# Kernel optimization log

Measured on AMD Instinct MI355X. Metric: run time of the kernel, lower is better.

The kernel has to match this reference:

```python
import jax, jax.numpy as jnp
import numpy as np

N_QUBITS = 14
CPLX = jnp.complex64


def _simulate(x, params):
    """Batched state-vector simulation of the QuantumGate circuit.

    x: (B, n) float angles for RX encoding; params: (2*n,) shared RY angles.
    Returns (B, n) Pauli-Z expectations.
    """
    n = N_QUBITS
    B = x.shape[0]
    dim = 2 ** n

    # RX(theta)|0> = [cos(theta/2), -i sin(theta/2)] per qubit -> product state.
    half = 0.5 * x
    c = jnp.cos(half).astype(CPLX)          # (B, n)
    s = jnp.sin(half).astype(CPLX)
    v = jnp.stack([c, -1j * s], axis=-1)     # (B, n, 2)

    state = jnp.ones((B, 1), dtype=CPLX)
    for q in range(n):  # fixed small loop over qubits; builds (B, 2^n)
        state = (state[:, :, None] * v[:, q, None, :]).reshape(B, -1)

    p = params.reshape(2, n)
    for layer in range(2):
        # RY rotations (shared angles across batch)
        for w in range(n):
            th = 0.5 * p[layer, w]
            cw, sw = jnp.cos(th), jnp.sin(th)
            G = jnp.stack([jnp.stack([cw, -sw]), jnp.stack([sw, cw])]).astype(CPLX)  # 2x2
            left, right = 2 ** w, 2 ** (n - w - 1)
            st = state.reshape(B, left, 2, right)
            state = jnp.einsum('ij,bljr->blir', G, st).reshape(B, dim)
        # CNOT chain on adjacent wires (w -> w+1)
        for w in range(n - 1):
            left, right = 2 ** w, 2 ** (n - w - 2)
            st = state.reshape(B, left, 2, 2, right)
            st = jnp.concatenate([st[:, :, 0:1], st[:, :, 1:2, ::-1]], axis=2)
            state = st.reshape(B, dim)

    probs = state.real ** 2 + state.imag ** 2  # (B, 2^n)
    outs = []
    for w in range(n):
        left, right = 2 ** w, 2 ** (n - w - 1)
        pr = probs.reshape(B, left, 2, right)
        outs.append(pr[:, :, 0].sum(axis=(1, 2)) - pr[:, :, 1].sum(axis=(1, 2)))
    return jnp.stack(outs, axis=1)  # (B, n)


def setup_inputs() -> dict:
    key = jax.random.key(0)
    k1, k2 = jax.random.split(key)
    x = jax.random.normal(k1, (4096, N_QUBITS), dtype=jnp.float32)
    params = jax.random.normal(k2, (2 * N_QUBITS,), dtype=jnp.float32)
    return {"x": x, "params": params}


def reference(x, params):
    return _simulate(x, params)
```

## Files before the change

### kernel.cpp

```cpp
#include <hip/hip_runtime.h>
#include <hip/hip_bf16.h>

#define NQ 14
#define BLOCK 64
#define ELEMS_PER_BLOCK (BLOCK / 8)


typedef float2 cplx;
__device__ __forceinline__ cplx cmul(cplx a, cplx b) {
    return make_float2(a.x * b.x - a.y * b.y, a.x * b.y + a.y * b.x);
}
__device__ __forceinline__ cplx cmadd(cplx acc, cplx a, cplx b) {
    return make_float2(acc.x + a.x * b.x - a.y * b.y,
                       acc.y + a.x * b.y + a.y * b.x);
}
__device__ __forceinline__ cplx conjc(cplx a) { return make_float2(a.x, -a.y); }
__device__ __forceinline__ cplx cscale(float s, cplx a) { return make_float2(s * a.x, s * a.y); }

__global__ __launch_bounds__(BLOCK) void qsim_tm(const void* __restrict__ xraw,
                                                 const void* __restrict__ praw,
                                                 void* __restrict__ outraw)
{
    const int tid  = threadIdx.x;
    const int lane = tid & 63;
    const int s    = lane & 7;
    const int g8   = lane & ~7;
    const int e  = (s >> 2) & 1;
    const int d  = (s >> 1) & 1;
    const int dp = s & 1;
    const int b  = blockIdx.x * ELEMS_PER_BLOCK + (tid >> 3);

    const unsigned short* hw = (const unsigned short*)xraw;
    int ev = 0;
    for (int k = 0; k < 64; ++k) {
        unsigned short v = hw[k];
        int ex = (v >> 7) & 0xFF;
        if (ex == 0xFF || ex > 140 || (ex != 0 && ex < 110)) ev++;
    }
    const int isbf = (ev < 8) ? 1 : 0;

    float c1a[NQ], s1a[NQ];
    cplx u0[NQ], u1[NQ];
    #pragma unroll
    for (int q = 0; q < NQ; ++q) {
        float p0, p1, xq;
        if (isbf) {
            p0 = (float)((const __hip_bfloat16*)praw)[q];
            p1 = (float)((const __hip_bfloat16*)praw)[NQ + q];
            xq = (float)((const __hip_bfloat16*)xraw)[b * NQ + q];
        } else {
            p0 = ((const float*)praw)[q];
            p1 = ((const float*)praw)[NQ + q];
            xq = ((const float*)xraw)[b * NQ + q];
        }
        float c0 = cosf(0.5f * p0), s0 = sinf(0.5f * p0);
        c1a[q] = cosf(0.5f * p1);
        s1a[q] = sinf(0.5f * p1);
        float rc = cosf(0.5f * xq), rs = sinf(0.5f * xq);
        u0[q] = make_float2(c0 * rc,  s0 * rs);
        u1[q] = make_float2(s0 * rc, -c0 * rs);
    }

    cplx L = make_float2((s == 0) ? 1.0f : 0.0f, 0.0f);
    cplx hist[NQ];
    #pragma unroll
    for (int q = 0; q < NQ; ++q) {
        float Lr[8], Li[8];
        #pragma unroll
        for (int sp = 0; sp < 8; ++sp) {
            Lr[sp] = __shfl(L.x, g8 + sp, 64);
            Li[sp] = __shfl(L.y, g8 + sp, 64);
        }
        const float c1 = c1a[q], s1 = s1a[q];
        const float gd0 = d  ? -s1 : c1;
        const float gd1 = d  ?  c1 : s1;
        const float gp0 = dp ? -s1 : c1;
        const float gp1 = dp ?  c1 : s1;
        const cplx ud    = d  ? u1[q] : u0[q];
        const cplx udx   = d  ? u0[q] : u1[q];
        const cplx updc  = conjc(dp ? u1[q] : u0[q]);
        const cplx updxc = conjc(dp ? u0[q] : u1[q]);

        cplx newL = make_float2(0.0f, 0.0f);
        #pragma unroll
        for (int ep = 0; ep < 2; ++ep) {
            const int f = e ^ ep;
            const float gg = (f == 0) ? (gd0 * gp0) : (gd1 * gp1);
            const int base = ep << 2;
            cplx in0 = cmadd(cmul(updc, make_float2(Lr[base + 0], Li[base + 0])),
                             updxc, make_float2(Lr[base + 1], Li[base + 1]));
            cplx in1 = cmadd(cmul(updc, make_float2(Lr[base + 2], Li[base + 2])),
                             updxc, make_float2(Lr[base + 3], Li[base + 3]));
            cplx mid = cmadd(cmul(ud, in0), udx, in1);
            newL = cmadd(newL, make_float2(gg, 0.0f), mid);
        }
        L = newL;
        hist[q] = L;
    }

    const float sgn = e ? -1.0f : 1.0f;
    cplx R = make_float2(1.0f, 0.0f);
    #pragma unroll
    for (int qq = 0; qq < NQ; ++qq) {
        const int q = NQ - 1 - qq;
        float t = sgn * (hist[q].x * R.x - hist[q].y * R.y);
        t += __shfl_xor(t, 1, 64);
        t += __shfl_xor(t, 2, 64);
        t += __shfl_xor(t, 4, 64);
        if (s == 0) {
            if (isbf) ((__hip_bfloat16*)outraw)[b * NQ + q] = __float2bfloat16(t);
            else      ((float*)outraw)[b * NQ + q] = t;
        }
        if (qq == NQ - 1) break;

        float Rr[8], Ri[8];
        #pragma unroll
        for (int sp = 0; sp < 8; ++sp) {
            Rr[sp] = __shfl(R.x, g8 + sp, 64);
            Ri[sp] = __shfl(R.y, g8 + sp, 64);
        }
        const float c1 = c1a[q], s1 = s1a[q];
        const cplx ud    = d  ? u1[q] : u0[q];
        const cplx udx   = d  ? u0[q] : u1[q];
        const cplx updc  = conjc(dp ? u1[q] : u0[q]);
        const cplx updxc = conjc(dp ? u0[q] : u1[q]);

        cplx newR = make_float2(0.0f, 0.0f);
        #pragma unroll
        for (int es = 0; es < 2; ++es) {
            const int f = es ^ e;
            const float g0 = (f == 0) ? c1 : s1;
            const float g1 = (f == 0) ? -s1 : c1;
            const cplx cb0 = cscale(g0, updc);
            const cplx cb1 = cscale(g1, updxc);
            const cplx ca0 = cscale(g0, ud);
            const cplx ca1 = cscale(g1, udx);
            const int base = es << 2;
            cplx ib0 = cmadd(cmul(cb0, make_float2(Rr[base + 0], Ri[base + 0])),
                             cb1, make_float2(Rr[base + 1], Ri[base + 1]));
            cplx ib1 = cmadd(cmul(cb0, make_float2(Rr[base + 2], Ri[base + 2])),
                             cb1, make_float2(Rr[base + 3], Ri[base + 3]));
            newR = cmadd(cmadd(newR, ca0, ib0), ca1, ib1);
        }
        R = newR;
    }
}

extern "C" void kernel_launch(void* const* d_in, const int* in_sizes, int n_in,
                              void* d_out, int out_size, void* d_ws, size_t ws_size,
                              hipStream_t stream) {
    const void* x = d_in[0];
    const void* params = d_in[1];
    const int B = in_sizes[0] / NQ;
    const int grid = B / ELEMS_PER_BLOCK;
    qsim_tm<<<grid, BLOCK, 0, stream>>>(x, params, d_out);
}
```

Measured before the change: 75.54 us.

## Factor transfer-matrix contraction into xor-shuffle butterflies with fast trig and larger blocks

Replaces the 16 indexed shuffles per qubit step in both the left and right sweeps with a staged butterfly of xor shuffles at distances 1, 2 and 4. The 8x8 transfer-matrix application is factored into per-index 2x2 steps, which cuts both shuffle and FMA count. It also vectorises the dtype-probe and x loads, switches to __sinf/__cosf intrinsics, and raises the block to 256 threads. The fast trig intrinsics lose some accuracy, and the bf16 detection threshold now samples 16 halfwords instead of 64.

```diff
diff --git a/kernel.cpp b/kernel.cpp
--- a/kernel.cpp
+++ b/kernel.cpp
@@ -2,61 +2,89 @@
 #include <hip/hip_bf16.h>
 
 #define NQ 14
-#define BLOCK 64
-#define ELEMS_PER_BLOCK (BLOCK / 8)
+#define BLOCK 256
+#define EPB (BLOCK / 8)
 
 
 typedef float2 cplx;
 __device__ __forceinline__ cplx cmul(cplx a, cplx b) {
     return make_float2(a.x * b.x - a.y * b.y, a.x * b.y + a.y * b.x);
 }
-__device__ __forceinline__ cplx cmadd(cplx acc, cplx a, cplx b) {
-    return make_float2(acc.x + a.x * b.x - a.y * b.y,
-                       acc.y + a.x * b.y + a.y * b.x);
+__device__ __forceinline__ cplx cconjmul(cplx a, cplx b) {
+    return make_float2(a.x * b.x + a.y * b.y, a.x * b.y - a.y * b.x);
 }
-__device__ __forceinline__ cplx conjc(cplx a) { return make_float2(a.x, -a.y); }
-__device__ __forceinline__ cplx cscale(float s, cplx a) { return make_float2(s * a.x, s * a.y); }
+__device__ __forceinline__ cplx shxor(cplx v, int m) {
+    return make_float2(__shfl_xor(v.x, m, 64), __shfl_xor(v.y, m, 64));
+}
 
-__global__ __launch_bounds__(BLOCK) void qsim_tm(const void* __restrict__ xraw,
-                                                 const void* __restrict__ praw,
-                                                 void* __restrict__ outraw)
+__global__ __launch_bounds__(BLOCK, 1) void qsim_tm2(const void* __restrict__ xraw,
+                                                     const void* __restrict__ praw,
+                                                     void* __restrict__ outraw)
 {
-    const int tid  = threadIdx.x;
-    const int lane = tid & 63;
-    const int s    = lane & 7;
-    const int g8   = lane & ~7;
-    const int e  = (s >> 2) & 1;
-    const int d  = (s >> 1) & 1;
-    const int dp = s & 1;
-    const int b  = blockIdx.x * ELEMS_PER_BLOCK + (tid >> 3);
+    const int tid = threadIdx.x;
+    const int s   = tid & 7;
+    const int e   = (s >> 2) & 1;
+    const int d   = (s >> 1) & 1;
+    const int p   = s & 1;
+    const int b   = blockIdx.x * EPB + (tid >> 3);
 
-    const unsigned short* hw = (const unsigned short*)xraw;
     int ev = 0;
-    for (int k = 0; k < 64; ++k) {
-        unsigned short v = hw[k];
-        int ex = (v >> 7) & 0xFF;
-        if (ex == 0xFF || ex > 140 || (ex != 0 && ex < 110)) ev++;
+    {
+        const uint4* sp4 = (const uint4*)xraw;
+        uint4 w[4];
+        #pragma unroll
+        for (int k = 0; k < 4; ++k) w[k] = sp4[k];
+        const unsigned* wu = (const unsigned*)w;
+        #pragma unroll
+        for (int k = 0; k < 8; ++k) {
+            unsigned v = wu[k];
+            #pragma unroll
+            for (int h = 0; h < 2; ++h) {
+                int ex = (v >> (7 + 16 * h)) & 0xFF;
+                ev += (ex == 0xFF || ex > 140 || (ex != 0 && ex < 110)) ? 1 : 0;
+            }
+        }
     }
-    const int isbf = (ev < 8) ? 1 : 0;
+    const bool isbf = (ev < 4);
+
+    float xang[NQ];
+    if (isbf) {
+        const unsigned* xu = (const unsigned*)xraw;
+        #pragma unroll
+        for (int k = 0; k < 7; ++k) {
+            unsigned v = xu[b * 7 + k];
+            unsigned lo = (v & 0xFFFFu) << 16;
+            unsigned hi = v & 0xFFFF0000u;
+            xang[2 * k]     = __uint_as_float(lo);
+            xang[2 * k + 1] = __uint_as_float(hi);
+        }
+    } else {
+        const float2* xf = (const float2*)xraw;
+        #pragma unroll
+        for (int k = 0; k < 7; ++k) {
+            float2 v = xf[b * 7 + k];
+            xang[2 * k]     = v.x;
+            xang[2 * k + 1] = v.y;
+        }
+    }
 
     float c1a[NQ], s1a[NQ];
     cplx u0[NQ], u1[NQ];
     #pragma unroll
     for (int q = 0; q < NQ; ++q) {
-        float p0, p1, xq;
+        float p0, p1;
         if (isbf) {
             p0 = (float)((const __hip_bfloat16*)praw)[q];
             p1 = (float)((const __hip_bfloat16*)praw)[NQ + q];
-            xq = (float)((const __hip_bfloat16*)xraw)[b * NQ + q];
         } else {
             p0 = ((const float*)praw)[q];
             p1 = ((const float*)praw)[NQ + q];
-            xq = ((const float*)xraw)[b * NQ + q];
         }
-        float c0 = cosf(0.5f * p0), s0 = sinf(0.5f * p0);
-        c1a[q] = cosf(0.5f * p1);
-        s1a[q] = sinf(0.5f * p1);
-        float rc = cosf(0.5f * xq), rs = sinf(0.5f * xq);
+        float a0 = 0.5f * p0, a1 = 0.5f * p1, ax = 0.5f * xang[q];
+        float c0 = __cosf(a0), s0 = __sinf(a0);
+        c1a[q] = __cosf(a1);
+        s1a[q] = __sinf(a1);
+        float rc = __cosf(ax), rs = __sinf(ax);
         u0[q] = make_float2(c0 * rc,  s0 * rs);
         u1[q] = make_float2(s0 * rc, -c0 * rs);
     }
@@ -65,36 +93,22 @@
     cplx hist[NQ];
     #pragma unroll
     for (int q = 0; q < NQ; ++q) {
-        float Lr[8], Li[8];
-        #pragma unroll
-        for (int sp = 0; sp < 8; ++sp) {
-            Lr[sp] = __shfl(L.x, g8 + sp, 64);
-            Li[sp] = __shfl(L.y, g8 + sp, 64);
-        }
+        const cplx u0q = u0[q], u1q = u1[q];
         const float c1 = c1a[q], s1 = s1a[q];
-        const float gd0 = d  ? -s1 : c1;
-        const float gd1 = d  ?  c1 : s1;
-        const float gp0 = dp ? -s1 : c1;
-        const float gp1 = dp ?  c1 : s1;
-        const cplx ud    = d  ? u1[q] : u0[q];
-        const cplx udx   = d  ? u0[q] : u1[q];
-        const cplx updc  = conjc(dp ? u1[q] : u0[q]);
-        const cplx updxc = conjc(dp ? u0[q] : u1[q]);
-
-        cplx newL = make_float2(0.0f, 0.0f);
-        #pragma unroll
-        for (int ep = 0; ep < 2; ++ep) {
-            const int f = e ^ ep;
-            const float gg = (f == 0) ? (gd0 * gp0) : (gd1 * gp1);
-            const int base = ep << 2;
-            cplx in0 = cmadd(cmul(updc, make_float2(Lr[base + 0], Li[base + 0])),
-                             updxc, make_float2(Lr[base + 1], Li[base + 1]));
-            cplx in1 = cmadd(cmul(updc, make_float2(Lr[base + 2], Li[base + 2])),
-                             updxc, make_float2(Lr[base + 3], Li[base + 3]));
-            cplx mid = cmadd(cmul(ud, in0), udx, in1);
-            newL = cmadd(newL, make_float2(gg, 0.0f), mid);
-        }
-        L = newL;
+        cplx Lx = shxor(L, 1);
+        cplx A = cconjmul(u0q, L);
+        cplx A2 = cconjmul(u1q, Lx);
+        A.x += A2.x; A.y += A2.y;
+        cplx Ax = shxor(A, 2);
+        cplx B = cmul(u0q, A);
+        cplx B2 = cmul(u1q, Ax);
+        B.x += B2.x; B.y += B2.y;
+        const float g0d = d ? -s1 : c1, g0p = p ? -s1 : c1;
+        const float g1d = d ?  c1 : s1, g1p = p ?  c1 : s1;
+        const float gg0 = g0d * g0p, gg1 = g1d * g1p;
+        cplx Bx = shxor(B, 4);
+        L.x = gg0 * B.x + gg1 * Bx.x;
+        L.y = gg0 * B.y + gg1 * Bx.y;
         hist[q] = L;
     }
 
@@ -113,36 +127,28 @@
         }
         if (qq == NQ - 1) break;
 
-        float Rr[8], Ri[8];
-        #pragma unroll
-        for (int sp = 0; sp < 8; ++sp) {
-            Rr[sp] = __shfl(R.x, g8 + sp, 64);
-            Ri[sp] = __shfl(R.y, g8 + sp, 64);
-        }
+        const cplx u0q = u0[q], u1q = u1[q];
         const float c1 = c1a[q], s1 = s1a[q];
-        const cplx ud    = d  ? u1[q] : u0[q];
-        const cplx udx   = d  ? u0[q] : u1[q];
-        const cplx updc  = conjc(dp ? u1[q] : u0[q]);
-        const cplx updxc = conjc(dp ? u0[q] : u1[q]);
-
-        cplx newR = make_float2(0.0f, 0.0f);
-        #pragma unroll
-        for (int es = 0; es < 2; ++es) {
-            const int f = es ^ e;
-            const float g0 = (f == 0) ? c1 : s1;
-            const float g1 = (f == 0) ? -s1 : c1;
-            const cplx cb0 = cscale(g0, updc);
-            const cplx cb1 = cscale(g1, updxc);
-            const cplx ca0 = cscale(g0, ud);
-            const cplx ca1 = cscale(g1, udx);
-            const int base = es << 2;
-            cplx ib0 = cmadd(cmul(cb0, make_float2(Rr[base + 0], Ri[base + 0])),
-                             cb1, make_float2(Rr[base + 1], Ri[base + 1]));
-            cplx ib1 = cmadd(cmul(cb0, make_float2(Rr[base + 2], Ri[base + 2])),
-                             cb1, make_float2(Rr[base + 3], Ri[base + 3]));
-            newR = cmadd(cmadd(newR, ca0, ib0), ca1, ib1);
-        }
-        R = newR;
+        cplx Rx = shxor(R, 1);
+        cplx t0 = cconjmul(u0q, R);
+        cplx t1 = cconjmul(u1q, Rx);
+        const float gp0 = p ? -s1 : c1, gp0x = p ?  c1 : -s1;
+        const float gp1 = p ?  c1 : s1, gp1x = p ?  s1 :  c1;
+        cplx P0 = make_float2(gp0 * t0.x + gp0x * t1.x, gp0 * t0.y + gp0x * t1.y);
+        cplx P1 = make_float2(gp1 * t0.x + gp1x * t1.x, gp1 * t0.y + gp1x * t1.y);
+        const float gd0 = d ? -s1 : c1, gd0x = d ?  c1 : -s1;
+        const float gd1 = d ?  c1 : s1, gd1x = d ?  s1 :  c1;
+        cplx P0x = shxor(P0, 2);
+        cplx P1x = shxor(P1, 2);
+        cplx m0  = cmul(u0q, P0);
+        cplx m0x = cmul(u1q, P0x);
+        cplx Q0 = make_float2(gd0 * m0.x + gd0x * m0x.x, gd0 * m0.y + gd0x * m0x.y);
+        cplx m1  = cmul(u0q, P1);
+        cplx m1x = cmul(u1q, P1x);
+        cplx Q1 = make_float2(gd1 * m1.x + gd1x * m1x.x, gd1 * m1.y + gd1x * m1x.y);
+        cplx Q1x = shxor(Q1, 4);
+        R.x = Q0.x + Q1x.x;
+        R.y = Q0.y + Q1x.y;
     }
 }
 
@@ -152,6 +158,6 @@
     const void* x = d_in[0];
     const void* params = d_in[1];
     const int B = in_sizes[0] / NQ;
-    const int grid = B / ELEMS_PER_BLOCK;
-    qsim_tm<<<grid, BLOCK, 0, stream>>>(x, params, d_out);
+    const int grid = (B * 8) / BLOCK;
+    qsim_tm2<<<grid, BLOCK, 0, stream>>>(x, params, d_out);
 }
```

Measured after the change: 62.09 us. -17.8%, faster.
